# Optimization experiments

Hardware: AMD Instinct MI355X
Metric: run time of the kernel (lower is better)

## Reference

```python
import jax, jax.numpy as jnp
import numpy as np

N = 500_000
N_ATOMS = 5
T = 8                # angle triplets per (residue, bead) table row
CONT_LEN = 36
GATE_OFFSET = 1
NUM_EXPERTS = 18
BEAD_COL = 36
MAX_BEADS = 4
ANGLE_WEIGHT = 1.0
EPS = 1e-8
MIN_LEN = 0.02


def setup_inputs() -> dict:
    key = jax.random.key(0)
    ks = jax.random.split(key, 8)
    x = jax.random.uniform(ks[0], (N, 38), dtype=jnp.float32)
    # gate column holds residue id in [1, num_experts]; bead column in [0, max_beads)
    res = jax.random.randint(ks[1], (N,), 1, NUM_EXPERTS + 1).astype(jnp.float32)
    bead = jax.random.randint(ks[2], (N,), 0, MAX_BEADS).astype(jnp.float32)
    x = x.at[:, CONT_LEN + 1].set(res)
    x = x.at[:, BEAD_COL].set(bead)
    y_true = jax.random.normal(ks[3], (N, N_ATOMS * 3), dtype=jnp.float32)
    y_pred = jax.random.normal(ks[4], (N, N_ATOMS * 3), dtype=jnp.float32)
    mask = (jax.random.uniform(ks[5], (N, N_ATOMS * 3)) < 0.85).astype(jnp.float32)
    # -1 entries act as invalid-triplet sentinels (trip_ok branch)
    trip = jax.random.randint(ks[6], (NUM_EXPERTS, MAX_BEADS, T, 3), -1, N_ATOMS, dtype=jnp.int32)
    valid = jax.random.randint(ks[7], (NUM_EXPERTS, MAX_BEADS, T), 0, 2, dtype=jnp.int32)
    return {"x": x, "y_true": y_true, "y_pred": y_pred, "mask": mask,
            "angle_triplets_table": trip, "angle_valid_table": valid}


def _atom_mse(true, pred, m):
    # masked per-atom squared error, normalized by count of valid atoms per sample
    se_atom = jnp.sum(jnp.square(true - pred) * m, axis=-1)          # [N, A]
    atom_valid = jnp.any(m > 0.0, axis=-1).astype(se_atom.dtype)     # [N, A]
    num = jnp.sum(se_atom * atom_valid, axis=-1)
    den = jnp.sum(atom_valid, axis=-1) + EPS
    return jnp.mean(num / den)


def _angle_loss(x, true, pred, m, trip_table, valid_table):
    gate = x[:, CONT_LEN + 1]
    gate = jnp.where(jnp.isfinite(gate), gate, 0.0)
    res_id = jnp.clip(jnp.round(gate).astype(jnp.int32) - GATE_OFFSET, 0, NUM_EXPERTS - 1)
    bead = x[:, BEAD_COL]
    bead = jnp.where(jnp.isfinite(bead), bead, 0.0)
    bead_id = jnp.clip(jnp.round(bead).astype(jnp.int32), 0, MAX_BEADS - 1)

    atom_valid = jnp.any(m > 0.0, axis=-1)                           # [N, A]
    trip = trip_table[res_id, bead_id]                               # [N, T, 3]
    base_valid = valid_table[res_id, bead_id]                        # [N, T]
    trip_ok = jnp.all(trip >= 0, axis=-1)
    ts = jnp.maximum(trip, 0)
    i_idx, j_idx, k_idx = ts[..., 0], ts[..., 1], ts[..., 2]         # [N, T]

    rows = jnp.arange(true.shape[0])[:, None]
    vi = atom_valid[rows, i_idx]
    vj = atom_valid[rows, j_idx]
    vk = atom_valid[rows, k_idx]
    ti, tj, tk = true[rows, i_idx], true[rows, j_idx], true[rows, k_idx]   # [N, T, 3]
    pi, pj, pk = pred[rows, i_idx], pred[rows, j_idx], pred[rows, k_idx]

    v1t, v2t, v1p, v2p = ti - tj, tk - tj, pi - pj, pk - pj
    ml2 = jnp.float32(MIN_LEN * MIN_LEN)
    sq = lambda v: jnp.sum(jnp.square(v), axis=-1)
    l1t2, l2t2, l1p2, l2p2 = sq(v1t), sq(v2t), sq(v1p), sq(v2p)

    valid = (trip_ok & (base_valid > 0) & vi & vj & vk
             & (l1t2 > ml2) & (l2t2 > ml2) & (l1p2 > ml2) & (l2p2 > ml2))

    unit = lambda v, l2: v * jax.lax.rsqrt(jnp.maximum(l2, ml2))[..., None]
    u1t, u2t = unit(v1t, l1t2), unit(v2t, l2t2)
    u1p, u2p = unit(v1p, l1p2), unit(v2p, l2p2)

    clip = lambda c: jnp.clip(c, -1.0 + 1e-6, 1.0 - 1e-6)
    cos_t = clip(jnp.sum(u1t * u2t, axis=-1))
    cos_p = clip(jnp.sum(u1p * u2p, axis=-1))
    sin_t = jnp.linalg.norm(jnp.cross(u1t, u2t), axis=-1)
    sin_p = jnp.linalg.norm(jnp.cross(u1p, u2p), axis=-1)

    per_ang = jnp.square(cos_p - cos_t) + jnp.square(sin_p - sin_t)
    per_ang = jnp.where(valid, per_ang, 0.0)
    num = jnp.sum(per_ang, axis=-1)
    den = jnp.sum(valid.astype(jnp.float32), axis=-1) + EPS
    return jnp.mean(num / den)


def reference(x, y_true, y_pred, mask, angle_triplets_table, angle_valid_table):
    true = y_true.reshape(-1, N_ATOMS, 3).astype(jnp.float32)
    pred = y_pred.reshape(-1, N_ATOMS, 3).astype(jnp.float32)
    m = mask.reshape(-1, N_ATOMS, 3).astype(jnp.float32)
    atom = _atom_mse(true, pred, m)
    ang = _angle_loss(x, true, pred, m, angle_triplets_table, angle_valid_table)
    return atom + ANGLE_WEIGHT * ang
```

## Files before the change

kernel.cpp:

```cpp
#include <hip/hip_runtime.h>
#include <math.h>

#define NATOMS 5
#define NEXP 18
#define NBEAD 4
#define EPSV 1e-8f
#define ML2 (0.02f * 0.02f)

__device__ __forceinline__ void sel5(const float* a, int idx, float& vx, float& vy, float& vz) {
    vx = a[0]; vy = a[1]; vz = a[2];
#pragma unroll
    for (int q = 1; q < 5; q++) {
        bool c = (idx == q);
        vx = c ? a[3 * q + 0] : vx;
        vy = c ? a[3 * q + 1] : vy;
        vz = c ? a[3 * q + 2] : vz;
    }
}

__global__ __launch_bounds__(256, 5) void loss_kernel(
    const float* __restrict__ xin, const float* __restrict__ y_true,
    const float* __restrict__ y_pred, const float* __restrict__ mask,
    const int* __restrict__ trip, const int* __restrict__ valid,
    float* __restrict__ out, int n, float inv_n) {
    __shared__ float sT[3840];
    __shared__ float sP[3840];
    __shared__ unsigned sMask[256];
    __shared__ unsigned sTbl[72][3];
    __shared__ float red[4];

    const int tid = threadIdx.x;

    sMask[tid] = 0u;
    if (tid < NEXP * NBEAD) {
        unsigned w0 = 0u, w1 = 0u, w2 = 0u;
#pragma unroll
        for (int t = 0; t < 8; t++) {
            int b = tid * 8 + t;
            int i = trip[b * 3 + 0], j = trip[b * 3 + 1], k = trip[b * 3 + 2];
            unsigned ok = (i >= 0 && j >= 0 && k >= 0 && valid[b] > 0) ? 1u : 0u;
            unsigned ic = (unsigned)min(max(i, 0), NATOMS - 1);
            unsigned jc = (unsigned)min(max(j, 0), NATOMS - 1);
            unsigned kc = (unsigned)min(max(k, 0), NATOMS - 1);
            unsigned e = ic | (jc << 3) | (kc << 6) | (ok << 9);
            if (t < 3) w0 |= e << (t * 10);
            else if (t < 6) w1 |= e << ((t - 3) * 10);
            else w2 |= e << ((t - 6) * 10);
        }
        sTbl[tid][0] = w0; sTbl[tid][1] = w1; sTbl[tid][2] = w2;
    }
    __syncthreads();

    const int row0 = blockIdx.x * 256;
    int rows = n - row0;
    if (rows > 256) rows = 256;
    const int cnt = rows * 15;
    const int cnt4 = cnt >> 2;
    const size_t base = (size_t)row0 * 15;

    const float4* gt = reinterpret_cast<const float4*>(y_true + base);
    const float4* gp = reinterpret_cast<const float4*>(y_pred + base);
    const float4* gm = reinterpret_cast<const float4*>(mask + base);
    for (int i = tid; i < cnt4; i += 256) {
        float4 t4 = gt[i];
        float4 p4 = gp[i];
        float4 m4 = gm[i];
        reinterpret_cast<float4*>(sT)[i] = t4;
        reinterpret_cast<float4*>(sP)[i] = p4;
        int e = i << 2;
        int r = e / 15;
        int p = e - r * 15;
        unsigned b0 = (m4.x > 0.f ? 1u : 0u) | (m4.y > 0.f ? 2u : 0u) |
                      (m4.z > 0.f ? 4u : 0u) | (m4.w > 0.f ? 8u : 0u);
        unsigned sh = b0 << p;
        unsigned lo = sh & 0x7fffu;
        unsigned hi = sh >> 15;
        atomicOr(&sMask[r], lo);
        if (hi) atomicOr(&sMask[r + 1], hi);
    }
    for (int i = (cnt4 << 2) + tid; i < cnt; i += 256) {
        sT[i] = y_true[base + i];
        sP[i] = y_pred[base + i];
        if (mask[base + i] > 0.f) {
            int r = i / 15;
            atomicOr(&sMask[r], 1u << (i - r * 15));
        }
    }
    __syncthreads();

    float result = 0.0f;
    const int row = row0 + tid;
    if (row < n) {
        float T[15], P[15];
        const float* st = sT + tid * 15;
        const float* sp = sP + tid * 15;
#pragma unroll
        for (int c = 0; c < 15; c++) { T[c] = st[c]; P[c] = sp[c]; }
        const unsigned mrow = sMask[tid];

        float num_a = 0.f, den_a = 0.f;
        int avm = 0;
#pragma unroll
        for (int a = 0; a < 5; a++) {
            unsigned mb = (mrow >> (3 * a)) & 7u;
            float se = 0.f;
#pragma unroll
            for (int c = 0; c < 3; c++) {
                float d = T[3 * a + c] - P[3 * a + c];
                se += ((mb >> c) & 1u) ? d * d : 0.f;
            }
            if (mb) { num_a += se; den_a += 1.f; avm |= (1 << a); }
        }
        result = num_a / (den_a + EPSV);

        float2 gb = *reinterpret_cast<const float2*>(xin + (size_t)row * 38 + 36);
        float bead = gb.x, gate = gb.y;
        gate = isfinite(gate) ? gate : 0.f;
        bead = isfinite(bead) ? bead : 0.f;
        gate = fminf(fmaxf(gate, -1e6f), 1e6f);
        bead = fminf(fmaxf(bead, -1e6f), 1e6f);
        int res_id = min(max((int)rintf(gate) - 1, 0), NEXP - 1);
        int bead_id = min(max((int)rintf(bead), 0), NBEAD - 1);
        int combo = res_id * NBEAD + bead_id;
        unsigned w0 = sTbl[combo][0], w1 = sTbl[combo][1], w2 = sTbl[combo][2];

        float num_g = 0.f, den_g = 0.f;
#pragma unroll
        for (int t = 0; t < 8; t++) {
            unsigned wrd = (t < 3) ? w0 : (t < 6) ? w1 : w2;
            int sh = (t < 3) ? t : (t < 6) ? (t - 3) : (t - 6);
            unsigned e = (wrd >> (sh * 10)) & 0x3ffu;
            int ii = e & 7, jj = (e >> 3) & 7, kk = (e >> 6) & 7;
            bool wok = ((e >> 9) & 1u) != 0u;

            float tix, tiy, tiz, tjx, tjy, tjz, tkx, tky, tkz;
            sel5(T, ii, tix, tiy, tiz);
            sel5(T, jj, tjx, tjy, tjz);
            sel5(T, kk, tkx, tky, tkz);
            float pix, piy, piz, pjx, pjy, pjz, pkx, pky, pkz;
            sel5(P, ii, pix, piy, piz);
            sel5(P, jj, pjx, pjy, pjz);
            sel5(P, kk, pkx, pky, pkz);

            float v1tx = tix - tjx, v1ty = tiy - tjy, v1tz = tiz - tjz;
            float v2tx = tkx - tjx, v2ty = tky - tjy, v2tz = tkz - tjz;
            float v1px = pix - pjx, v1py = piy - pjy, v1pz = piz - pjz;
            float v2px = pkx - pjx, v2py = pky - pjy, v2pz = pkz - pjz;

            float l1t = fmaf(v1tx, v1tx, fmaf(v1ty, v1ty, v1tz * v1tz));
            float l2t = fmaf(v2tx, v2tx, fmaf(v2ty, v2ty, v2tz * v2tz));
            float l1p = fmaf(v1px, v1px, fmaf(v1py, v1py, v1pz * v1pz));
            float l2p = fmaf(v2px, v2px, fmaf(v2py, v2py, v2pz * v2pz));

            bool valid = wok && ((avm >> ii) & 1) && ((avm >> jj) & 1) && ((avm >> kk) & 1) &&
                         (l1t > ML2) && (l2t > ML2) && (l1p > ML2) && (l2p > ML2);

            float rt = __builtin_amdgcn_rsqf(fmaxf(l1t, ML2) * fmaxf(l2t, ML2));
            float rp = __builtin_amdgcn_rsqf(fmaxf(l1p, ML2) * fmaxf(l2p, ML2));

            float dott = fmaf(v1tx, v2tx, fmaf(v1ty, v2ty, v1tz * v2tz));
            float dotp = fmaf(v1px, v2px, fmaf(v1py, v2py, v1pz * v2pz));
            float cut = dott * rt;
            float cup = dotp * rp;
            float cost = fminf(fmaxf(cut, -1.f + 1e-6f), 1.f - 1e-6f);
            float cosp = fminf(fmaxf(cup, -1.f + 1e-6f), 1.f - 1e-6f);
            float s2t = fmaxf(fmaf(-cut, cut, 1.f), 0.f);
            float s2p = fmaxf(fmaf(-cup, cup, 1.f), 0.f);
            float sint = __builtin_amdgcn_sqrtf(s2t);
            float sinp = __builtin_amdgcn_sqrtf(s2p);

            float dc = cosp - cost, dsn = sinp - sint;
            if (valid) { num_g += fmaf(dc, dc, dsn * dsn); den_g += 1.f; }
        }
        result += num_g / (den_g + EPSV);
    }

#pragma unroll
    for (int off = 32; off > 0; off >>= 1)
        result += __shfl_down(result, off, 64);
    int lane = tid & 63, wv = tid >> 6;
    if (lane == 0) red[wv] = result;
    __syncthreads();
    if (tid == 0) {
        float s = red[0] + red[1] + red[2] + red[3];
        atomicAdd(out, s * inv_n);
    }
}

extern "C" void kernel_launch(void* const* d_in, const int* in_sizes, int n_in,
                              void* d_out, int out_size, void* d_ws, size_t ws_size,
                              hipStream_t stream) {
    const float* x = (const float*)d_in[0];
    const float* y_true = (const float*)d_in[1];
    const float* y_pred = (const float*)d_in[2];
    const float* mask = (const float*)d_in[3];
    const int* trip = (const int*)d_in[4];
    const int* valid = (const int*)d_in[5];
    float* out = (float*)d_out;

    const int n = in_sizes[1] / 15;

    hipMemsetAsync(out, 0, sizeof(float), stream);
    const int blocks = (n + 255) / 256;
    loss_kernel<<<blocks, 256, 0, stream>>>(x, y_true, y_pred, mask, trip, valid, out, n,
                                            1.0f / (float)n);
}
```

Measured before the change: 193.9 us.

## Use direct global-to-LDS loads, flat mask bitfield, and offset-based LDS gathers

Loads y_true/y_pred tiles into shared memory with global_load_lds instead of staging through registers. The mask is packed into a flat shared bitfield with fewer atomics and no per-element division by 15. The triplet table now stores precomputed atom offsets, so coordinates are read directly from LDS instead of through select chains over register arrays. This cuts VALU and register pressure but adds dynamically indexed LDS reads and an extra barrier.

Measured after the change: 195.3 us. No clear change (+0.7%).

```diff
diff --git a/kernel.cpp b/kernel.cpp
--- a/kernel.cpp
+++ b/kernel.cpp
@@ -1,22 +1,13 @@
 #include <hip/hip_runtime.h>
 #include <math.h>
 
-#define NATOMS 5
 #define NEXP 18
 #define NBEAD 4
 #define EPSV 1e-8f
 #define ML2 (0.02f * 0.02f)
 
-__device__ __forceinline__ void sel5(const float* a, int idx, float& vx, float& vy, float& vz) {
-    vx = a[0]; vy = a[1]; vz = a[2];
-#pragma unroll
-    for (int q = 1; q < 5; q++) {
-        bool c = (idx == q);
-        vx = c ? a[3 * q + 0] : vx;
-        vy = c ? a[3 * q + 1] : vy;
-        vz = c ? a[3 * q + 2] : vz;
-    }
-}
+#define AS1U(p) ((const __attribute__((address_space(1))) unsigned*)(p))
+#define AS3U(p) ((__attribute__((address_space(3))) unsigned*)(p))
 
 __global__ __launch_bounds__(256, 5) void loss_kernel(
     const float* __restrict__ xin, const float* __restrict__ y_true,
@@ -25,29 +16,29 @@
     float* __restrict__ out, int n, float inv_n) {
     __shared__ float sT[3840];
     __shared__ float sP[3840];
-    __shared__ unsigned sMask[256];
-    __shared__ unsigned sTbl[72][3];
-    __shared__ float red[4];
+    __shared__ unsigned sBits[124];
+    __shared__ unsigned sTbl[72][4];
 
     const int tid = threadIdx.x;
+    const int lane = tid & 63;
+    const int wv = tid >> 6;
 
-    sMask[tid] = 0u;
+    if (tid < 124) sBits[tid] = 0u;
     if (tid < NEXP * NBEAD) {
-        unsigned w0 = 0u, w1 = 0u, w2 = 0u;
+        unsigned w[4] = {0u, 0u, 0u, 0u};
 #pragma unroll
         for (int t = 0; t < 8; t++) {
             int b = tid * 8 + t;
             int i = trip[b * 3 + 0], j = trip[b * 3 + 1], k = trip[b * 3 + 2];
             unsigned ok = (i >= 0 && j >= 0 && k >= 0 && valid[b] > 0) ? 1u : 0u;
-            unsigned ic = (unsigned)min(max(i, 0), NATOMS - 1);
-            unsigned jc = (unsigned)min(max(j, 0), NATOMS - 1);
-            unsigned kc = (unsigned)min(max(k, 0), NATOMS - 1);
-            unsigned e = ic | (jc << 3) | (kc << 6) | (ok << 9);
-            if (t < 3) w0 |= e << (t * 10);
-            else if (t < 6) w1 |= e << ((t - 3) * 10);
-            else w2 |= e << ((t - 6) * 10);
+            unsigned oi = 3u * (unsigned)min(max(i, 0), 4);
+            unsigned oj = 3u * (unsigned)min(max(j, 0), 4);
+            unsigned ov = 3u * (unsigned)min(max(k, 0), 4);
+            unsigned e = oi | (oj << 4) | (ov << 8) | (ok << 12);
+            w[t >> 1] |= e << ((t & 1) * 16);
         }
-        sTbl[tid][0] = w0; sTbl[tid][1] = w1; sTbl[tid][2] = w2;
+        sTbl[tid][0] = w[0]; sTbl[tid][1] = w[1];
+        sTbl[tid][2] = w[2]; sTbl[tid][3] = w[3];
     }
     __syncthreads();
 
@@ -57,90 +48,88 @@
     const int cnt = rows * 15;
     const int cnt4 = cnt >> 2;
     const size_t base = (size_t)row0 * 15;
+    const float4* gt = (const float4*)(y_true + base);
+    const float4* gp = (const float4*)(y_pred + base);
+    const float4* gm = (const float4*)(mask + base);
+    float4* sT4 = (float4*)sT;
+    float4* sP4 = (float4*)sP;
 
-    const float4* gt = reinterpret_cast<const float4*>(y_true + base);
-    const float4* gp = reinterpret_cast<const float4*>(y_pred + base);
-    const float4* gm = reinterpret_cast<const float4*>(mask + base);
-    for (int i = tid; i < cnt4; i += 256) {
-        float4 t4 = gt[i];
-        float4 p4 = gp[i];
-        float4 m4 = gm[i];
-        reinterpret_cast<float4*>(sT)[i] = t4;
-        reinterpret_cast<float4*>(sP)[i] = p4;
-        int e = i << 2;
-        int r = e / 15;
-        int p = e - r * 15;
-        unsigned b0 = (m4.x > 0.f ? 1u : 0u) | (m4.y > 0.f ? 2u : 0u) |
-                      (m4.z > 0.f ? 4u : 0u) | (m4.w > 0.f ? 8u : 0u);
-        unsigned sh = b0 << p;
-        unsigned lo = sh & 0x7fffu;
-        unsigned hi = sh >> 15;
-        atomicOr(&sMask[r], lo);
-        if (hi) atomicOr(&sMask[r + 1], hi);
+    for (int ib = wv * 64; ib + 64 <= cnt4; ib += 256) {
+        __builtin_amdgcn_global_load_lds(AS1U(gt + ib + lane), AS3U(sT4 + ib), 16, 0, 0);
+        __builtin_amdgcn_global_load_lds(AS1U(gp + ib + lane), AS3U(sP4 + ib), 16, 0, 0);
     }
+    for (int i = (cnt4 & ~63) + tid; i < cnt4; i += 256) { sT4[i] = gt[i]; sP4[i] = gp[i]; }
     for (int i = (cnt4 << 2) + tid; i < cnt; i += 256) {
         sT[i] = y_true[base + i];
         sP[i] = y_pred[base + i];
-        if (mask[base + i] > 0.f) {
-            int r = i / 15;
-            atomicOr(&sMask[r], 1u << (i - r * 15));
+    }
+
+    for (int i = tid; i < cnt4; i += 256) {
+        float4 m4 = gm[i];
+        unsigned b0 = (m4.x > 0.f ? 1u : 0u) | (m4.y > 0.f ? 2u : 0u) |
+                      (m4.z > 0.f ? 4u : 0u) | (m4.w > 0.f ? 8u : 0u);
+        if (b0) {
+            int e = i << 2;
+            unsigned long long v = (unsigned long long)b0 << (e & 31);
+            atomicOr(&sBits[e >> 5], (unsigned)v);
+            unsigned hi = (unsigned)(v >> 32);
+            if (hi) atomicOr(&sBits[(e >> 5) + 1], hi);
         }
+    }
+    for (int i = (cnt4 << 2) + tid; i < cnt; i += 256) {
+        if (mask[base + i] > 0.f) atomicOr(&sBits[i >> 5], 1u << (i & 31));
     }
     __syncthreads();
 
     float result = 0.0f;
     const int row = row0 + tid;
     if (row < n) {
-        float T[15], P[15];
         const float* st = sT + tid * 15;
         const float* sp = sP + tid * 15;
-#pragma unroll
-        for (int c = 0; c < 15; c++) { T[c] = st[c]; P[c] = sp[c]; }
-        const unsigned mrow = sMask[tid];
+        const int bb = tid * 15;
+        unsigned long long mw =
+            ((unsigned long long)sBits[(bb >> 5) + 1] << 32) | sBits[bb >> 5];
+        const unsigned mrow = (unsigned)((mw >> (bb & 31)) & 0x7fffu);
 
         float num_a = 0.f, den_a = 0.f;
-        int avm = 0;
+        unsigned avm2 = 0u;
 #pragma unroll
         for (int a = 0; a < 5; a++) {
             unsigned mb = (mrow >> (3 * a)) & 7u;
-            float se = 0.f;
-#pragma unroll
-            for (int c = 0; c < 3; c++) {
-                float d = T[3 * a + c] - P[3 * a + c];
-                se += ((mb >> c) & 1u) ? d * d : 0.f;
-            }
-            if (mb) { num_a += se; den_a += 1.f; avm |= (1 << a); }
+            float d0 = st[3 * a + 0] - sp[3 * a + 0];
+            float d1 = st[3 * a + 1] - sp[3 * a + 1];
+            float d2 = st[3 * a + 2] - sp[3 * a + 2];
+            float se = (mb & 1u ? d0 * d0 : 0.f) + (mb & 2u ? d1 * d1 : 0.f) +
+                       (mb & 4u ? d2 * d2 : 0.f);
+            if (mb) { num_a += se; den_a += 1.f; avm2 |= 1u << (3 * a); }
         }
         result = num_a / (den_a + EPSV);
 
-        float2 gb = *reinterpret_cast<const float2*>(xin + (size_t)row * 38 + 36);
-        float bead = gb.x, gate = gb.y;
-        gate = isfinite(gate) ? gate : 0.f;
-        bead = isfinite(bead) ? bead : 0.f;
-        gate = fminf(fmaxf(gate, -1e6f), 1e6f);
-        bead = fminf(fmaxf(bead, -1e6f), 1e6f);
-        int res_id = min(max((int)rintf(gate) - 1, 0), NEXP - 1);
-        int bead_id = min(max((int)rintf(bead), 0), NBEAD - 1);
+        float2 gb = *(const float2*)(xin + (size_t)row * 38 + 36);
+        float beadf = isfinite(gb.x) ? gb.x : 0.f;
+        float gatef = isfinite(gb.y) ? gb.y : 0.f;
+        gatef = fminf(fmaxf(gatef, -1e6f), 1e6f);
+        beadf = fminf(fmaxf(beadf, -1e6f), 1e6f);
+        int res_id = min(max((int)rintf(gatef) - 1, 0), NEXP - 1);
+        int bead_id = min(max((int)rintf(beadf), 0), NBEAD - 1);
         int combo = res_id * NBEAD + bead_id;
-        unsigned w0 = sTbl[combo][0], w1 = sTbl[combo][1], w2 = sTbl[combo][2];
+        unsigned tw0 = sTbl[combo][0], tw1 = sTbl[combo][1];
+        unsigned tw2 = sTbl[combo][2], tw3 = sTbl[combo][3];
 
         float num_g = 0.f, den_g = 0.f;
 #pragma unroll
         for (int t = 0; t < 8; t++) {
-            unsigned wrd = (t < 3) ? w0 : (t < 6) ? w1 : w2;
-            int sh = (t < 3) ? t : (t < 6) ? (t - 3) : (t - 6);
-            unsigned e = (wrd >> (sh * 10)) & 0x3ffu;
-            int ii = e & 7, jj = (e >> 3) & 7, kk = (e >> 6) & 7;
-            bool wok = ((e >> 9) & 1u) != 0u;
+            unsigned wrd = (t < 2) ? tw0 : (t < 4) ? tw1 : (t < 6) ? tw2 : tw3;
+            unsigned e = (wrd >> ((t & 1) * 16)) & 0xffffu;
+            int oi = e & 15, oj = (e >> 4) & 15, ov = (e >> 8) & 15;
+            bool wok = ((e >> 12) & 1u) != 0u;
 
-            float tix, tiy, tiz, tjx, tjy, tjz, tkx, tky, tkz;
-            sel5(T, ii, tix, tiy, tiz);
-            sel5(T, jj, tjx, tjy, tjz);
-            sel5(T, kk, tkx, tky, tkz);
-            float pix, piy, piz, pjx, pjy, pjz, pkx, pky, pkz;
-            sel5(P, ii, pix, piy, piz);
-            sel5(P, jj, pjx, pjy, pjz);
-            sel5(P, kk, pkx, pky, pkz);
+            float tix = st[oi], tiy = st[oi + 1], tiz = st[oi + 2];
+            float tjx = st[oj], tjy = st[oj + 1], tjz = st[oj + 2];
+            float tkx = st[ov], tky = st[ov + 1], tkz = st[ov + 2];
+            float pix = sp[oi], piy = sp[oi + 1], piz = sp[oi + 2];
+            float pjx = sp[oj], pjy = sp[oj + 1], pjz = sp[oj + 2];
+            float pkx = sp[ov], pky = sp[ov + 1], pkz = sp[ov + 2];
 
             float v1tx = tix - tjx, v1ty = tiy - tjy, v1tz = tiz - tjz;
             float v2tx = tkx - tjx, v2ty = tky - tjy, v2tz = tkz - tjz;
@@ -152,8 +141,9 @@
             float l1p = fmaf(v1px, v1px, fmaf(v1py, v1py, v1pz * v1pz));
             float l2p = fmaf(v2px, v2px, fmaf(v2py, v2py, v2pz * v2pz));
 
-            bool valid = wok && ((avm >> ii) & 1) && ((avm >> jj) & 1) && ((avm >> kk) & 1) &&
-                         (l1t > ML2) && (l2t > ML2) && (l1p > ML2) && (l2p > ML2);
+            bool okv = wok && ((avm2 >> oi) & 1) && ((avm2 >> oj) & 1) &&
+                       ((avm2 >> ov) & 1) && (l1t > ML2) && (l2t > ML2) &&
+                       (l1p > ML2) && (l2p > ML2);
 
             float rt = __builtin_amdgcn_rsqf(fmaxf(l1t, ML2) * fmaxf(l2t, ML2));
             float rp = __builtin_amdgcn_rsqf(fmaxf(l1p, ML2) * fmaxf(l2p, ML2));
@@ -164,27 +154,23 @@
             float cup = dotp * rp;
             float cost = fminf(fmaxf(cut, -1.f + 1e-6f), 1.f - 1e-6f);
             float cosp = fminf(fmaxf(cup, -1.f + 1e-6f), 1.f - 1e-6f);
-            float s2t = fmaxf(fmaf(-cut, cut, 1.f), 0.f);
-            float s2p = fmaxf(fmaf(-cup, cup, 1.f), 0.f);
-            float sint = __builtin_amdgcn_sqrtf(s2t);
-            float sinp = __builtin_amdgcn_sqrtf(s2p);
+            float sint = __builtin_amdgcn_sqrtf(fmaxf(fmaf(-cut, cut, 1.f), 0.f));
+            float sinp = __builtin_amdgcn_sqrtf(fmaxf(fmaf(-cup, cup, 1.f), 0.f));
 
             float dc = cosp - cost, dsn = sinp - sint;
-            if (valid) { num_g += fmaf(dc, dc, dsn * dsn); den_g += 1.f; }
+            if (okv) { num_g += fmaf(dc, dc, dsn * dsn); den_g += 1.f; }
         }
         result += num_g / (den_g + EPSV);
     }
 
+    __syncthreads();
 #pragma unroll
     for (int off = 32; off > 0; off >>= 1)
         result += __shfl_down(result, off, 64);
-    int lane = tid & 63, wv = tid >> 6;
+    float* red = (float*)sBits;
     if (lane == 0) red[wv] = result;
     __syncthreads();
-    if (tid == 0) {
-        float s = red[0] + red[1] + red[2] + red[3];
-        atomicAdd(out, s * inv_n);
-    }
+    if (tid == 0) atomicAdd(out, (red[0] + red[1] + red[2] + red[3]) * inv_n);
 }
 
 extern "C" void kernel_launch(void* const* d_in, const int* in_sizes, int n_in,
```
